# Kernel optimization log

Measured on AMD Instinct MI355X. Metric: run time of the kernel, lower is better.

## Reference

```python
import jax, jax.numpy as jnp
import numpy as np

D_MODEL = 1024
HIDDEN = 4096
N_EXPERTS = 8
TOP_K = 2


def setup_inputs() -> dict:
    key = jax.random.key(0)
    ks = jax.random.split(key, 7)
    x = jax.random.normal(ks[0], (4, 2048, D_MODEL), dtype=jnp.float32)
    s = 0.02
    Wg = jax.random.normal(ks[1], (D_MODEL, N_EXPERTS), dtype=jnp.float32) * s
    bg = jnp.zeros((N_EXPERTS,), dtype=jnp.float32)
    W1 = jax.random.normal(ks[2], (N_EXPERTS, D_MODEL, HIDDEN), dtype=jnp.float32) * s
    b1 = jnp.zeros((N_EXPERTS, HIDDEN), dtype=jnp.float32)
    W2 = jax.random.normal(ks[3], (N_EXPERTS, HIDDEN, D_MODEL), dtype=jnp.float32) * s
    b2 = jnp.zeros((N_EXPERTS, D_MODEL), dtype=jnp.float32)
    return {"x": x, "Wg": Wg, "bg": bg, "W1": W1, "b1": b1, "W2": W2, "b2": b2}


def reference(x, Wg, bg, W1, b1, W2, b2):
    B, T, D = x.shape
    xf = x.reshape(-1, D)                      # (N, D)
    N = xf.shape[0]

    # --- top-k gate ---
    logits = xf @ Wg + bg                      # (N, E)
    all_probs = jax.nn.softmax(logits, axis=-1)
    topk_logits, topk_idx = jax.lax.top_k(logits, TOP_K)   # (N, k)
    topk_gates = jax.nn.softmax(topk_logits, axis=-1)      # (N, k), sums to 1

    # scatter gates into dense (N, E) masks (matches torch scatter_add_)
    rows = jnp.arange(N)[:, None]
    gate_mask = jnp.zeros((N, N_EXPERTS), dtype=xf.dtype).at[rows, topk_idx].add(topk_gates)
    dispatch_mask = jnp.zeros((N, N_EXPERTS), dtype=xf.dtype).at[rows, topk_idx].add(1.0)

    # --- experts: dense batched form; unselected tokens have gate 0 so math matches ---
    h = jnp.einsum('nd,edh->neh', xf, W1) + b1             # (N, E, H)
    h = jax.nn.relu(h)
    y = jnp.einsum('neh,ehd->ned', h, W2) + b2             # (N, E, D)
    out = jnp.einsum('ned,ne->nd', y, gate_mask)           # weighted combine
    outputs = out.reshape(B, T, D)

    # --- load-balance loss + metadata ---
    tokens_per_expert = (dispatch_mask > 0).sum(axis=0)
    assignment_fraction = gate_mask.sum(axis=0) / N
    expected_prob = all_probs.mean(axis=0)
    load_balance_loss = (expected_prob * assignment_fraction).sum() * N_EXPERTS

    return (outputs, load_balance_loss, tokens_per_expert, expected_prob, assignment_fraction)
```

## Files before the change

### kernel.cpp

```cpp
#include <hip/hip_runtime.h>
#include <stdint.h>

#define D_MODEL 1024
#define HID     4096
#define NE      8
#define NTOK    8192
#define NSLOT   (NTOK*2)
#define TM      128
#define MAX_RB  136
#define MPAD    (MAX_RB*TM)
#define HHALF   2048
#define GATE_BLOCKS 32

typedef unsigned short u16;
typedef __attribute__((ext_vector_type(8))) __bf16 bf16x8;
typedef __attribute__((ext_vector_type(4))) float  f32x4;

__device__ __forceinline__ u16 f2bu(float f){
  uint32_t u = __builtin_bit_cast(uint32_t, f);
  uint32_t r = (u + 0x7FFFu + ((u >> 16) & 1u)) >> 16;
  return (u16)r;
}

__device__ __forceinline__ void gload16(const u16* src, u16* lds){
  __builtin_amdgcn_global_load_lds((const __attribute__((address_space(1))) void*)src,
                                   (__attribute__((address_space(3))) void*)lds, 16, 0, 0);
}

__global__ __launch_bounds__(256) void xcvt_kernel(const float* __restrict__ x, u16* __restrict__ x16){
  size_t i = (size_t)blockIdx.x*256 + threadIdx.x;
  const float4* p = (const float4*)(x + i*8);
  float4 a = p[0], b = p[1];
  u16 o[8] = {f2bu(a.x),f2bu(a.y),f2bu(a.z),f2bu(a.w),f2bu(b.x),f2bu(b.y),f2bu(b.z),f2bu(b.w)};
  *(int4*)(x16 + i*8) = *(int4*)o;
}

__global__ __launch_bounds__(256) void transpose_cvt(const float* __restrict__ in,
                                                     u16* __restrict__ out, int R, int C)
{
  __shared__ float tile[32][33];
  int e = blockIdx.z;
  int r0 = blockIdx.y * 32, c0 = blockIdx.x * 32;
  const float* src = in + (size_t)e * R * C;
  u16* dst = out + (size_t)e * R * C;
  int tx = threadIdx.x, ty = threadIdx.y;
#pragma unroll
  for (int i = 0; i < 4; i++){
    int r = r0 + ty + i*8;
    tile[ty + i*8][tx] = src[(size_t)r * C + c0 + tx];
  }
  __syncthreads();
#pragma unroll
  for (int i = 0; i < 4; i++){
    int c = c0 + ty + i*8;
    dst[(size_t)c * R + r0 + tx] = f2bu(tile[tx][ty + i*8]);
  }
}

__global__ __launch_bounds__(256) void gate_kernel(
    const float* __restrict__ x, const float* __restrict__ Wg, const float* __restrict__ bg,
    int* __restrict__ topk, float* __restrict__ gates,
    float* __restrict__ part_probs, float* __restrict__ part_assign, int* __restrict__ part_cnt)
{
  __shared__ float sp[256][8];
  __shared__ float sa[256][8];
  __shared__ int   sc[256][8];
  int t = threadIdx.x;
  int n = blockIdx.x * 256 + t;
  float lg[8];
#pragma unroll
  for (int e = 0; e < 8; e++) lg[e] = bg[e];
  const float4* xr = (const float4*)(x + (size_t)n * D_MODEL);
  for (int j = 0; j < D_MODEL/4; j++){
    float4 v = xr[j];
    const float* wr = Wg + (size_t)j * 32;
#pragma unroll
    for (int e = 0; e < 8; e++)
      lg[e] += v.x*wr[e] + v.y*wr[8+e] + v.z*wr[16+e] + v.w*wr[24+e];
  }
  float m = lg[0];
#pragma unroll
  for (int e = 1; e < 8; e++) m = fmaxf(m, lg[e]);
  float p[8]; float s = 0.f;
#pragma unroll
  for (int e = 0; e < 8; e++){ p[e] = expf(lg[e]-m); s += p[e]; }
  float inv = 1.f / s;
  int bi = 0; float best = lg[0];
#pragma unroll
  for (int e = 1; e < 8; e++) if (lg[e] > best){ best = lg[e]; bi = e; }
  int bi2 = 0; float best2 = -3.0e38f;
#pragma unroll
  for (int e = 0; e < 8; e++) if (e != bi && lg[e] > best2){ best2 = lg[e]; bi2 = e; }
  float t1 = expf(best2 - best);
  float g0 = 1.f / (1.f + t1);
  float g1 = t1 / (1.f + t1);
  topk[2*n] = bi;  topk[2*n+1] = bi2;
  gates[2*n] = g0; gates[2*n+1] = g1;
#pragma unroll
  for (int e = 0; e < 8; e++){
    sp[t][e] = p[e] * inv;
    sa[t][e] = (e == bi) ? g0 : ((e == bi2) ? g1 : 0.f);
    sc[t][e] = (e == bi || e == bi2) ? 1 : 0;
  }
  __syncthreads();
  if (t < 8){
    float s2 = 0.f; for (int i = 0; i < 256; i++) s2 += sp[i][t];
    part_probs[blockIdx.x*8 + t] = s2;
  } else if (t < 16){
    int e = t - 8; float s2 = 0.f; for (int i = 0; i < 256; i++) s2 += sa[i][e];
    part_assign[blockIdx.x*8 + e] = s2;
  } else if (t < 24){
    int e = t - 16; int c = 0; for (int i = 0; i < 256; i++) c += sc[i][e];
    part_cnt[blockIdx.x*8 + e] = c;
  }
}

__global__ __launch_bounds__(256) void scan_kernel(const int* __restrict__ part_cnt,
                                                   int* __restrict__ counts,
                                                   int* __restrict__ padded_off,
                                                   int* __restrict__ cursor,
                                                   int* __restrict__ block_expert,
                                                   int* __restrict__ routed)
{
  __shared__ int off[NE+1];
  int t = threadIdx.x;
  if (t == 0){
    int o = 0; off[0] = 0;
    for (int e = 0; e < NE; e++){
      int c = 0;
      for (int b = 0; b < GATE_BLOCKS; b++) c += part_cnt[b*8 + e];
      counts[e] = c;
      o += ((c + TM - 1) / TM) * TM;
      off[e+1] = o;
    }
    for (int e = 0; e <= NE; e++) padded_off[e] = off[e];
  }
  __syncthreads();
  if (t < NE) cursor[t] = 0;
  for (int rb = t; rb < MAX_RB; rb += 256){
    int e = -1;
    int r = rb * TM;
    for (int j = 0; j < NE; j++)
      if (r >= off[j] && r < off[j+1]) e = j;
    block_expert[rb] = e;
  }
  for (int i = t; i < MPAD; i += 256) routed[i] = -1;
}

__global__ __launch_bounds__(256) void place_kernel(const int* __restrict__ topk,
                                                    const int* __restrict__ padded_off,
                                                    int* __restrict__ cursor,
                                                    int* __restrict__ routed)
{
  int s = blockIdx.x * 256 + threadIdx.x;
  int e = topk[s];
  int pos = padded_off[e] + atomicAdd(&cursor[e], 1);
  routed[pos] = s;
}

__global__ __launch_bounds__(256) void gemm1_kernel(
    const u16* __restrict__ x16, const u16* __restrict__ w1t, const float* __restrict__ b1,
    const int* __restrict__ routed, const int* __restrict__ block_expert,
    u16* __restrict__ h, int half)
{
  int rb = blockIdx.y;
  int e = block_expert[rb];
  if (e < 0) return;
  __shared__ __align__(16) u16 Al[128][32];
  __shared__ __align__(16) u16 Bl[128][32];
  int t = threadIdx.x, cb = blockIdx.x;
  int lane = t & 63, wid = t >> 6;

  int srow0 = wid*32 + (lane >> 2);
  int srow1 = srow0 + 16;
  int sch = (lane & 3) * 8;

  int slot0 = routed[rb*TM + srow0];
  int slot1 = routed[rb*TM + srow1];
  int tok0 = slot0 >= 0 ? (slot0 >> 1) : 0;
  int tok1 = slot1 >= 0 ? (slot1 >> 1) : 0;
  const u16* srcA0 = x16 + (size_t)tok0 * D_MODEL + sch;
  const u16* srcA1 = x16 + (size_t)tok1 * D_MODEL + sch;
  const u16* wb = w1t + ((size_t)e*HID + (size_t)half*HHALF + (size_t)cb*128) * D_MODEL + sch;
  const u16* srcB0 = wb + (size_t)srow0 * D_MODEL;
  const u16* srcB1 = wb + (size_t)srow1 * D_MODEL;
  u16* lA0 = &Al[wid*32][0];
  u16* lA1 = &Al[wid*32 + 16][0];
  u16* lB0 = &Bl[wid*32][0];
  u16* lB1 = &Bl[wid*32 + 16][0];

  int wr = wid >> 1, wc = wid & 1;
  int fr = lane & 15, fk = lane >> 4;
  f32x4 acc[4][4];
#pragma unroll
  for (int i = 0; i < 4; i++)
#pragma unroll
    for (int j = 0; j < 4; j++) acc[i][j] = (f32x4){0.f,0.f,0.f,0.f};

  for (int k = 0; k < D_MODEL; k += 32){
    __syncthreads();
    gload16(srcA0 + k, lA0);
    gload16(srcA1 + k, lA1);
    gload16(srcB0 + k, lB0);
    gload16(srcB1 + k, lB1);
    __syncthreads();
    bf16x8 af[4], bf[4];
#pragma unroll
    for (int mm = 0; mm < 4; mm++) af[mm] = *(const bf16x8*)(&Al[wr*64 + mm*16 + fr][fk*8]);
#pragma unroll
    for (int nn = 0; nn < 4; nn++) bf[nn] = *(const bf16x8*)(&Bl[wc*64 + nn*16 + fr][fk*8]);
#pragma unroll
    for (int mm = 0; mm < 4; mm++)
#pragma unroll
      for (int nn = 0; nn < 4; nn++)
        acc[mm][nn] = __builtin_amdgcn_mfma_f32_16x16x32_bf16(af[mm], bf[nn], acc[mm][nn], 0, 0, 0);
  }
  int r4 = fk * 4;
#pragma unroll
  for (int nn = 0; nn < 4; nn++){
    int ct = wc*64 + nn*16 + fr;
    float bias = b1[(size_t)e*HID + (size_t)half*HHALF + cb*128 + ct];
#pragma unroll
    for (int mm = 0; mm < 4; mm++){
#pragma unroll
      for (int r = 0; r < 4; r++){
        int rt = wr*64 + mm*16 + r4 + r;
        float v = acc[mm][nn][r] + bias;
        v = v > 0.f ? v : 0.f;
        h[(size_t)(rb*TM + rt) * HHALF + cb*128 + ct] = f2bu(v);
      }
    }
  }
}

__global__ __launch_bounds__(256) void gemm2_kernel(
    const u16* __restrict__ h, const u16* __restrict__ w2t,
    const int* __restrict__ routed, const int* __restrict__ block_expert,
    const float* __restrict__ gates, float* __restrict__ y, int half)
{
  int rb = blockIdx.y;
  int e = block_expert[rb];
  if (e < 0) return;
  __shared__ __align__(16) u16 Al[128][32];
  __shared__ __align__(16) u16 Bl[128][32];
  __shared__ int   rslot[128];
  __shared__ float rgate[128];
  int t = threadIdx.x, cb = blockIdx.x;
  int lane = t & 63, wid = t >> 6;
  if (t < 128){
    int s = routed[rb*TM + t];
    rslot[t] = s;
    rgate[t] = (s >= 0) ? gates[s] : 0.f;
  }

  int srow0 = wid*32 + (lane >> 2);
  int srow1 = srow0 + 16;
  int sch = (lane & 3) * 8;
  const u16* srcA0 = h + (size_t)(rb*TM + srow0) * HHALF + sch;
  const u16* srcA1 = h + (size_t)(rb*TM + srow1) * HHALF + sch;
  const u16* wb = w2t + ((size_t)e*D_MODEL + (size_t)cb*128) * HID + (size_t)half*HHALF + sch;
  const u16* srcB0 = wb + (size_t)srow0 * HID;
  const u16* srcB1 = wb + (size_t)srow1 * HID;
  u16* lA0 = &Al[wid*32][0];
  u16* lA1 = &Al[wid*32 + 16][0];
  u16* lB0 = &Bl[wid*32][0];
  u16* lB1 = &Bl[wid*32 + 16][0];

  int wr = wid >> 1, wc = wid & 1;
  int fr = lane & 15, fk = lane >> 4;
  f32x4 acc[4][4];
#pragma unroll
  for (int i = 0; i < 4; i++)
#pragma unroll
    for (int j = 0; j < 4; j++) acc[i][j] = (f32x4){0.f,0.f,0.f,0.f};

  for (int k = 0; k < HHALF; k += 32){
    __syncthreads();
    gload16(srcA0 + k, lA0);
    gload16(srcA1 + k, lA1);
    gload16(srcB0 + k, lB0);
    gload16(srcB1 + k, lB1);
    __syncthreads();
    bf16x8 af[4], bf[4];
#pragma unroll
    for (int mm = 0; mm < 4; mm++) af[mm] = *(const bf16x8*)(&Al[wr*64 + mm*16 + fr][fk*8]);
#pragma unroll
    for (int nn = 0; nn < 4; nn++) bf[nn] = *(const bf16x8*)(&Bl[wc*64 + nn*16 + fr][fk*8]);
#pragma unroll
    for (int mm = 0; mm < 4; mm++)
#pragma unroll
      for (int nn = 0; nn < 4; nn++)
        acc[mm][nn] = __builtin_amdgcn_mfma_f32_16x16x32_bf16(af[mm], bf[nn], acc[mm][nn], 0, 0, 0);
  }
  int r4 = fk * 4;
#pragma unroll
  for (int mm = 0; mm < 4; mm++){
#pragma unroll
    for (int r = 0; r < 4; r++){
      int rt = wr*64 + mm*16 + r4 + r;
      int slot = rslot[rt];
      if (slot < 0) continue;
      float g = rgate[rt];
#pragma unroll
      for (int nn = 0; nn < 4; nn++){
        int ct = wc*64 + nn*16 + fr;
        size_t idx = (size_t)slot * D_MODEL + cb*128 + ct;
        float val = g * acc[mm][nn][r];
        if (half == 0) y[idx] = val;
        else           y[idx] += val;
      }
    }
  }
}

__global__ __launch_bounds__(256) void combine_kernel(
    const float* __restrict__ y, const int* __restrict__ topk, const float* __restrict__ gates,
    const float* __restrict__ b2, float* __restrict__ out)
{
  int i = blockIdx.x * 256 + threadIdx.x;
  int n = i >> 8;
  int d = (i & 255) * 4;
  float4 a  = *(const float4*)(y + (size_t)(2*n)   * D_MODEL + d);
  float4 b  = *(const float4*)(y + (size_t)(2*n+1) * D_MODEL + d);
  int e0 = topk[2*n], e1 = topk[2*n+1];
  float g0 = gates[2*n], g1 = gates[2*n+1];
  float4 c0 = *(const float4*)(b2 + (size_t)e0 * D_MODEL + d);
  float4 c1 = *(const float4*)(b2 + (size_t)e1 * D_MODEL + d);
  float4 o;
  o.x = a.x + b.x + g0*c0.x + g1*c1.x;
  o.y = a.y + b.y + g0*c0.y + g1*c1.y;
  o.z = a.z + b.z + g0*c0.z + g1*c1.z;
  o.w = a.w + b.w + g0*c0.w + g1*c1.w;
  *(float4*)(out + (size_t)n * D_MODEL + d) = o;
}

__global__ void finalize_kernel(const float* __restrict__ part_probs,
                                const float* __restrict__ part_assign,
                                const int* __restrict__ counts,
                                float* __restrict__ out_tail)
{
  __shared__ float ep[8], af[8];
  int t = threadIdx.x;
  if (t < 8){
    float s = 0.f;
    for (int b = 0; b < GATE_BLOCKS; b++) s += part_probs[b*8 + t];
    ep[t] = s / (float)NTOK;
  } else if (t < 16){
    int e = t - 8; float s = 0.f;
    for (int b = 0; b < GATE_BLOCKS; b++) s += part_assign[b*8 + e];
    af[e] = s / (float)NTOK;
  }
  __syncthreads();
  if (t == 0){
    float loss = 0.f;
    for (int e = 0; e < 8; e++) loss += ep[e] * af[e];
    out_tail[0] = loss * (float)NE;
  }
  if (t < 8){
    out_tail[1 + t]  = (float)counts[t];
    out_tail[9 + t]  = ep[t];
    out_tail[17 + t] = af[t];
  }
}

extern "C" void kernel_launch(void* const* d_in, const int* in_sizes, int n_in,
                              void* d_out, int out_size, void* d_ws, size_t ws_size,
                              hipStream_t stream)
{
  const float* x  = (const float*)d_in[0];
  const float* Wg = (const float*)d_in[1];
  const float* bg = (const float*)d_in[2];
  const float* W1 = (const float*)d_in[3];
  const float* b1 = (const float*)d_in[4];
  const float* W2 = (const float*)d_in[5];
  const float* b2 = (const float*)d_in[6];
  float* out = (float*)d_out;

  char* ws = (char*)d_ws;
  size_t o = 0;
  auto alloc = [&](size_t bytes) -> char* {
    char* p = ws + o; o = (o + bytes + 255) & ~(size_t)255; return p;
  };
  int*   topk        = (int*)   alloc((size_t)NSLOT*4);
  float* gates       = (float*) alloc((size_t)NSLOT*4);
  int*   counts      = (int*)   alloc(NE*4);
  int*   padded_off  = (int*)   alloc((NE+1)*4);
  int*   cursor      = (int*)   alloc(NE*4);
  int*   block_exp   = (int*)   alloc(MAX_RB*4);
  int*   routed      = (int*)   alloc((size_t)MPAD*4);
  float* part_probs  = (float*) alloc(GATE_BLOCKS*8*4);
  float* part_assign = (float*) alloc(GATE_BLOCKS*8*4);
  int*   part_cnt    = (int*)   alloc(GATE_BLOCKS*8*4);
  u16*   x16         = (u16*)   alloc((size_t)NTOK*D_MODEL*2);
  u16*   w1t         = (u16*)   alloc((size_t)NE*HID*D_MODEL*2);
  u16*   w2t         = (u16*)   alloc((size_t)NE*HID*D_MODEL*2);
  u16*   hbuf        = (u16*)   alloc((size_t)MPAD*HHALF*2);
  float* ybuf        = (float*) alloc((size_t)NSLOT*D_MODEL*4);
  (void)ws_size; (void)in_sizes; (void)n_in; (void)out_size;

  transpose_cvt<<<dim3(HID/32, D_MODEL/32, NE), dim3(32,8), 0, stream>>>(W1, w1t, D_MODEL, HID);
  transpose_cvt<<<dim3(D_MODEL/32, HID/32, NE), dim3(32,8), 0, stream>>>(W2, w2t, HID, D_MODEL);
  xcvt_kernel<<<(NTOK*D_MODEL)/(256*8), 256, 0, stream>>>(x, x16);
  gate_kernel<<<GATE_BLOCKS, 256, 0, stream>>>(x, Wg, bg, topk, gates, part_probs, part_assign, part_cnt);
  scan_kernel<<<1, 256, 0, stream>>>(part_cnt, counts, padded_off, cursor, block_exp, routed);
  place_kernel<<<NSLOT/256, 256, 0, stream>>>(topk, padded_off, cursor, routed);
  for (int half = 0; half < 2; half++){
    gemm1_kernel<<<dim3(HHALF/128, MAX_RB), 256, 0, stream>>>(x16, w1t, b1, routed, block_exp, hbuf, half);
    gemm2_kernel<<<dim3(D_MODEL/128, MAX_RB), 256, 0, stream>>>(hbuf, w2t, routed, block_exp, gates, ybuf, half);
  }
  combine_kernel<<<NTOK, 256, 0, stream>>>(ybuf, topk, gates, b2, out);
  finalize_kernel<<<1, 64, 0, stream>>>(part_probs, part_assign, counts, out + (size_t)NTOK*D_MODEL);
}
```

Measured before the change: 751.9 us.

## Double-buffer LDS tiles in expert GEMMs and swizzle blocks across XCDs

Both expert GEMM kernels now use two LDS buffers, so the async global-to-LDS load of the next K-slice is issued before the MFMA work on the current slice, and there is one barrier per slice instead of two. The 2D grid is flattened to 1D and remapped with an XCD-aware swizzle, so blocks sharing a row block land on the same XCD and can reuse its L2. LDS use per block doubles, and the swizzle assumes the grid size divides evenly by 8.

```diff
diff --git a/kernel.cpp b/kernel.cpp
--- a/kernel.cpp
+++ b/kernel.cpp
@@ -25,6 +25,11 @@
 __device__ __forceinline__ void gload16(const u16* src, u16* lds){
   __builtin_amdgcn_global_load_lds((const __attribute__((address_space(1))) void*)src,
                                    (__attribute__((address_space(3))) void*)lds, 16, 0, 0);
+}
+
+__device__ __forceinline__ int xcd_swz(int w, int nwg){
+  int q = nwg >> 3;
+  return (w & 7) * q + (w >> 3);
 }
 
 __global__ __launch_bounds__(256) void xcvt_kernel(const float* __restrict__ x, u16* __restrict__ x16){
@@ -163,12 +168,13 @@
     const int* __restrict__ routed, const int* __restrict__ block_expert,
     u16* __restrict__ h, int half)
 {
-  int rb = blockIdx.y;
+  int l = xcd_swz(blockIdx.x, gridDim.x);
+  int rb = l >> 4, cb = l & 15;
   int e = block_expert[rb];
   if (e < 0) return;
-  __shared__ __align__(16) u16 Al[128][32];
-  __shared__ __align__(16) u16 Bl[128][32];
-  int t = threadIdx.x, cb = blockIdx.x;
+  __shared__ __align__(16) u16 Al[2][128][32];
+  __shared__ __align__(16) u16 Bl[2][128][32];
+  int t = threadIdx.x;
   int lane = t & 63, wid = t >> 6;
 
   int srow0 = wid*32 + (lane >> 2);
@@ -184,10 +190,6 @@
   const u16* wb = w1t + ((size_t)e*HID + (size_t)half*HHALF + (size_t)cb*128) * D_MODEL + sch;
   const u16* srcB0 = wb + (size_t)srow0 * D_MODEL;
   const u16* srcB1 = wb + (size_t)srow1 * D_MODEL;
-  u16* lA0 = &Al[wid*32][0];
-  u16* lA1 = &Al[wid*32 + 16][0];
-  u16* lB0 = &Bl[wid*32][0];
-  u16* lB1 = &Bl[wid*32 + 16][0];
 
   int wr = wid >> 1, wc = wid & 1;
   int fr = lane & 15, fk = lane >> 4;
@@ -197,24 +199,35 @@
 #pragma unroll
     for (int j = 0; j < 4; j++) acc[i][j] = (f32x4){0.f,0.f,0.f,0.f};
 
-  for (int k = 0; k < D_MODEL; k += 32){
+#define STAGE1(bi, kk) do{ \
+    gload16(srcA0 + (kk), &Al[bi][wid*32][0]); \
+    gload16(srcA1 + (kk), &Al[bi][wid*32+16][0]); \
+    gload16(srcB0 + (kk), &Bl[bi][wid*32][0]); \
+    gload16(srcB1 + (kk), &Bl[bi][wid*32+16][0]); } while(0)
+
+#define COMPUTE1(bi) do{ \
+    bf16x8 af[4], bf[4]; \
+    _Pragma("unroll") \
+    for (int mm = 0; mm < 4; mm++) af[mm] = *(const bf16x8*)(&Al[bi][wr*64 + mm*16 + fr][fk*8]); \
+    _Pragma("unroll") \
+    for (int nn = 0; nn < 4; nn++) bf[nn] = *(const bf16x8*)(&Bl[bi][wc*64 + nn*16 + fr][fk*8]); \
+    _Pragma("unroll") \
+    for (int mm = 0; mm < 4; mm++) \
+      _Pragma("unroll") \
+      for (int nn = 0; nn < 4; nn++) \
+        acc[mm][nn] = __builtin_amdgcn_mfma_f32_16x16x32_bf16(af[mm], bf[nn], acc[mm][nn], 0, 0, 0); } while(0)
+
+  STAGE1(0, 0);
+  __syncthreads();
+  for (int k = 0; k < D_MODEL; k += 64){
+    STAGE1(1, k + 32);
+    COMPUTE1(0);
     __syncthreads();
-    gload16(srcA0 + k, lA0);
-    gload16(srcA1 + k, lA1);
-    gload16(srcB0 + k, lB0);
-    gload16(srcB1 + k, lB1);
+    if (k + 64 < D_MODEL) STAGE1(0, k + 64);
+    COMPUTE1(1);
     __syncthreads();
-    bf16x8 af[4], bf[4];
-#pragma unroll
-    for (int mm = 0; mm < 4; mm++) af[mm] = *(const bf16x8*)(&Al[wr*64 + mm*16 + fr][fk*8]);
-#pragma unroll
-    for (int nn = 0; nn < 4; nn++) bf[nn] = *(const bf16x8*)(&Bl[wc*64 + nn*16 + fr][fk*8]);
-#pragma unroll
-    for (int mm = 0; mm < 4; mm++)
-#pragma unroll
-      for (int nn = 0; nn < 4; nn++)
-        acc[mm][nn] = __builtin_amdgcn_mfma_f32_16x16x32_bf16(af[mm], bf[nn], acc[mm][nn], 0, 0, 0);
-  }
+  }
+
   int r4 = fk * 4;
 #pragma unroll
   for (int nn = 0; nn < 4; nn++){
@@ -231,6 +244,8 @@
       }
     }
   }
+#undef STAGE1
+#undef COMPUTE1
 }
 
 __global__ __launch_bounds__(256) void gemm2_kernel(
@@ -238,14 +253,15 @@
     const int* __restrict__ routed, const int* __restrict__ block_expert,
     const float* __restrict__ gates, float* __restrict__ y, int half)
 {
-  int rb = blockIdx.y;
+  int l = xcd_swz(blockIdx.x, gridDim.x);
+  int rb = l >> 3, cb = l & 7;
   int e = block_expert[rb];
   if (e < 0) return;
-  __shared__ __align__(16) u16 Al[128][32];
-  __shared__ __align__(16) u16 Bl[128][32];
+  __shared__ __align__(16) u16 Al[2][128][32];
+  __shared__ __align__(16) u16 Bl[2][128][32];
   __shared__ int   rslot[128];
   __shared__ float rgate[128];
-  int t = threadIdx.x, cb = blockIdx.x;
+  int t = threadIdx.x;
   int lane = t & 63, wid = t >> 6;
   if (t < 128){
     int s = routed[rb*TM + t];
@@ -261,10 +277,6 @@
   const u16* wb = w2t + ((size_t)e*D_MODEL + (size_t)cb*128) * HID + (size_t)half*HHALF + sch;
   const u16* srcB0 = wb + (size_t)srow0 * HID;
   const u16* srcB1 = wb + (size_t)srow1 * HID;
-  u16* lA0 = &Al[wid*32][0];
-  u16* lA1 = &Al[wid*32 + 16][0];
-  u16* lB0 = &Bl[wid*32][0];
-  u16* lB1 = &Bl[wid*32 + 16][0];
 
   int wr = wid >> 1, wc = wid & 1;
   int fr = lane & 15, fk = lane >> 4;
@@ -274,24 +286,35 @@
 #pragma unroll
     for (int j = 0; j < 4; j++) acc[i][j] = (f32x4){0.f,0.f,0.f,0.f};
 
-  for (int k = 0; k < HHALF; k += 32){
+#define STAGE2(bi, kk) do{ \
+    gload16(srcA0 + (kk), &Al[bi][wid*32][0]); \
+    gload16(srcA1 + (kk), &Al[bi][wid*32+16][0]); \
+    gload16(srcB0 + (kk), &Bl[bi][wid*32][0]); \
+    gload16(srcB1 + (kk), &Bl[bi][wid*32+16][0]); } while(0)
+
+#define COMPUTE2(bi) do{ \
+    bf16x8 af[4], bf[4]; \
+    _Pragma("unroll") \
+    for (int mm = 0; mm < 4; mm++) af[mm] = *(const bf16x8*)(&Al[bi][wr*64 + mm*16 + fr][fk*8]); \
+    _Pragma("unroll") \
+    for (int nn = 0; nn < 4; nn++) bf[nn] = *(const bf16x8*)(&Bl[bi][wc*64 + nn*16 + fr][fk*8]); \
+    _Pragma("unroll") \
+    for (int mm = 0; mm < 4; mm++) \
+      _Pragma("unroll") \
+      for (int nn = 0; nn < 4; nn++) \
+        acc[mm][nn] = __builtin_amdgcn_mfma_f32_16x16x32_bf16(af[mm], bf[nn], acc[mm][nn], 0, 0, 0); } while(0)
+
+  STAGE2(0, 0);
+  __syncthreads();
+  for (int k = 0; k < HHALF; k += 64){
+    STAGE2(1, k + 32);
+    COMPUTE2(0);
     __syncthreads();
-    gload16(srcA0 + k, lA0);
-    gload16(srcA1 + k, lA1);
-    gload16(srcB0 + k, lB0);
-    gload16(srcB1 + k, lB1);
+    if (k + 64 < HHALF) STAGE2(0, k + 64);
+    COMPUTE2(1);
     __syncthreads();
-    bf16x8 af[4], bf[4];
-#pragma unroll
-    for (int mm = 0; mm < 4; mm++) af[mm] = *(const bf16x8*)(&Al[wr*64 + mm*16 + fr][fk*8]);
-#pragma unroll
-    for (int nn = 0; nn < 4; nn++) bf[nn] = *(const bf16x8*)(&Bl[wc*64 + nn*16 + fr][fk*8]);
-#pragma unroll
-    for (int mm = 0; mm < 4; mm++)
-#pragma unroll
-      for (int nn = 0; nn < 4; nn++)
-        acc[mm][nn] = __builtin_amdgcn_mfma_f32_16x16x32_bf16(af[mm], bf[nn], acc[mm][nn], 0, 0, 0);
-  }
+  }
+
   int r4 = fk * 4;
 #pragma unroll
   for (int mm = 0; mm < 4; mm++){
@@ -311,6 +334,8 @@
       }
     }
   }
+#undef STAGE2
+#undef COMPUTE2
 }
 
 __global__ __launch_bounds__(256) void combine_kernel(
@@ -405,8 +430,8 @@
   scan_kernel<<<1, 256, 0, stream>>>(part_cnt, counts, padded_off, cursor, block_exp, routed);
   place_kernel<<<NSLOT/256, 256, 0, stream>>>(topk, padded_off, cursor, routed);
   for (int half = 0; half < 2; half++){
-    gemm1_kernel<<<dim3(HHALF/128, MAX_RB), 256, 0, stream>>>(x16, w1t, b1, routed, block_exp, hbuf, half);
-    gemm2_kernel<<<dim3(D_MODEL/128, MAX_RB), 256, 0, stream>>>(hbuf, w2t, routed, block_exp, gates, ybuf, half);
+    gemm1_kernel<<<16*MAX_RB, 256, 0, stream>>>(x16, w1t, b1, routed, block_exp, hbuf, half);
+    gemm2_kernel<<<8*MAX_RB, 256, 0, stream>>>(hbuf, w2t, routed, block_exp, gates, ybuf, half);
   }
   combine_kernel<<<NTOK, 256, 0, stream>>>(ybuf, topk, gates, b2, out);
   finalize_kernel<<<1, 64, 0, stream>>>(part_probs, part_assign, counts, out + (size_t)NTOK*D_MODEL);
```

Result: no change. 754.7 us (+0.4%).
